# Performance work log

Measured on AMD Instinct MI355X. Metric: run time of the kernel, lower is better.

## Reference

```python
import jax, jax.numpy as jnp
import numpy as np

N_S, N_H, N_ACT, N_LINKS = 512, 256, 7, 9
AXIS_LIST = jnp.array([2, 0, 2, 2, 2, 0, 2])
LINK_LIST = jnp.arange(N_ACT)
ROT_SIGN = jnp.array([1., 1., 1., 1., -1., 1., 1.], dtype=jnp.float32)  # rot[..., 4] *= -1
MASS = jnp.array([105.98, 105.98, 314.98, 279.2, 105.98, 105.98, 243.66], dtype=jnp.float32)
TOTAL_MASS = jnp.sum(MASS) + 100000.0 + 243.66
DIAGS = jnp.array([[12.19, 12.19, 3.061], [12.19, 12.19, 3.061], [15.41, 2094.71, 2103.19],
                   [9.522, 1966.28, 1966.28], [8.305, 3.061, 8.0386], [12.13, 12.13, 3.061],
                   [9.336, 44.41, 44.41]], dtype=jnp.float32)
INERTIAL = DIAGS[:, :, None] * jnp.eye(3, dtype=jnp.float32)          # (7,3,3) diagonal inertias
SUM_MASS = jnp.cumsum(MASS[::-1])[::-1].reshape(1, 1, 1, N_ACT)       # suffix sums
SUM_INERTIAL = jnp.cumsum(INERTIAL[::-1], axis=0)[::-1]               # (7,3,3)
TRIL = jnp.tril(jnp.ones((N_ACT, N_ACT), dtype=jnp.float32)).reshape(1, 1, N_ACT, 1, N_ACT)
MASS_MASK = MASS.reshape(1, 1, N_ACT, 1, 1) * TRIL                    # mass_H_wphi_mask
TF0 = jnp.array([[1, 0, 0, 0], [0, -1, 0, 0], [0, 0, 1.3, 6], [0, 0, 0, 1]], dtype=jnp.float32)
COM0 = jnp.array([[1, 0, 0, 0], [0, 1, 0, 0], [0, 0, 1, 0.5], [0, 0, 0, 1]], dtype=jnp.float32)
BASE_COM = (TF0 @ COM0)[:3, 3] * 243.66 / (100000.0 + 243.66)


def _skew(p):
    x, y, z = p[..., 0], p[..., 1], p[..., 2]
    z0 = jnp.zeros_like(x)
    return jnp.stack([jnp.stack([z0, -z, y], -1),
                      jnp.stack([z, z0, -x], -1),
                      jnp.stack([-y, x, z0], -1)], -2)


def _skew_mul(p):
    x, y, z = p[..., 0], p[..., 1], p[..., 2]
    r2 = x * x + y * y + z * z
    row0 = jnp.stack([r2 - x * x, -x * y, -x * z], -1)
    row1 = jnp.stack([-x * y, r2 - y * y, -y * z], -1)
    row2 = jnp.stack([-x * z, -y * z, r2 - z * z], -1)
    return jnp.stack([row0, row1, row2], -2)


def _inv3(H):
    a, b, c = H[..., 0, 0], H[..., 0, 1], H[..., 0, 2]
    d, e, f = H[..., 1, 0], H[..., 1, 1], H[..., 1, 2]
    g, h, i = H[..., 2, 0], H[..., 2, 1], H[..., 2, 2]
    det = a * (e * i - f * h) - b * (d * i - f * g) + c * (d * h - e * g)
    C11 = e * i - f * h; C12 = -(b * i - c * h); C13 = b * f - c * e
    C21 = -(d * i - f * g); C22 = a * i - c * g; C23 = -(a * f - c * d)
    C31 = d * h - e * g; C32 = -(a * h - b * g); C33 = a * e - b * d
    adj = jnp.stack([jnp.stack([C11, C21, C31], -1),
                     jnp.stack([C12, C22, C32], -1),
                     jnp.stack([C13, C23, C33], -1)], -2)
    return adj / det[..., None, None]


def _forward(com_list, link_pose_list, bm):
    rot = link_pose_list[:, :, :3, AXIS_LIST, LINK_LIST] * ROT_SIGN  # (n,h,3,7)
    if bm:
        del_p = com_list[:, :, :, :N_ACT] - link_pose_list[:, :, :3, 3, :N_ACT]  # (n,h,3,7)
        del_p_a = jnp.swapaxes(del_p, -1, -2)                                     # (n,h,7,3)
        del_p_skew = _skew(del_p_a)                                               # (n,h,7,3,3)
        jacob_t = jnp.cross(rot, del_p, axis=2)                                   # (n,h,3,7)
        jacob_tw = jacob_t * SUM_MASS
        H_w = jnp.sum(INERTIAL.reshape(1, 1, N_ACT, 3, 3)
                      + MASS.reshape(1, 1, N_ACT, 1, 1) * _skew_mul(del_p_a), axis=2)  # (n,h,3,3)
        term1 = jnp.einsum('aij,shja->shia', SUM_INERTIAL, rot)                   # (n,h,3,7)
        jac_w = jacob_t[:, :, None] * MASS_MASK                                   # (n,h,7,3,7)
        term2 = jnp.einsum('shaij,shajk->shik', del_p_skew, jac_w)                # (n,h,3,7)
        H_wphi = term1 + term2
        system_com = jnp.einsum('ntci,i->ntc', com_list, MASS) / TOTAL_MASS       # (n,h,3)
        r_og = _skew(system_com - BASE_COM)                                       # (n,h,3,3)
        H_s = TOTAL_MASS * (r_og @ r_og) + H_w
        H_theta = H_wphi - r_og @ jacob_tw
        H_inv = _inv3(H_s)
        top = -(jacob_tw / TOTAL_MASS + r_og @ (H_inv @ H_theta))
        bot = -(H_inv @ H_theta)
        return jnp.concatenate([top, bot], axis=2)                                # (n,h,6,7)
    else:
        del_p = link_pose_list[:, :, :3, 3, -2][..., None] - link_pose_list[:, :, :3, 3, :N_ACT]
        jt = jnp.cross(rot, del_p, axis=2)
        return jnp.concatenate([jt, rot], axis=2)


def setup_inputs() -> dict:
    key = jax.random.key(0)
    k1, k2 = jax.random.split(key)
    com_list = jax.random.normal(k1, (N_S, N_H, 3, N_ACT), dtype=jnp.float32)
    link_pose_list = jax.random.normal(k2, (N_S, N_H, 4, 4, N_LINKS), dtype=jnp.float32)
    return {"com_list": com_list, "link_pose_list": link_pose_list, "bm": 1}


def reference(com_list, link_pose_list, bm):
    return _forward(com_list, link_pose_list, bm)
```

## Files before the change

kernel.cpp:

```cpp
#include <hip/hip_runtime.h>


#define BLK 256

__global__ __launch_bounds__(BLK) void canadarm_jacob_kernel(
    const float* __restrict__ com,
    const float* __restrict__ pose,
    const int* __restrict__ bm_ptr,
    float* __restrict__ out,
    int n_items)
{
    __shared__ float lds[BLK * 42];

    const int tid = threadIdx.x;
    const int idx = blockIdx.x * BLK + tid;

    const float MASS[7] = {105.98f, 105.98f, 314.98f, 279.2f, 105.98f, 105.98f, 243.66f};
    const float SUMM[7] = {1261.76f, 1155.78f, 1049.80f, 734.82f, 455.62f, 349.64f, 243.66f};
    const float SIX[7] = {79.083f, 66.893f, 54.703f, 39.293f, 29.771f, 21.466f, 9.336f};
    const float SIY[7] = {4144.971f, 4132.781f, 4120.591f, 2025.881f, 59.601f, 56.540f, 44.410f};
    const float SIZ[7] = {4131.1016f, 4128.0406f, 4124.9796f, 2021.7896f, 55.5096f, 47.471f, 44.410f};
    const float TM     = 101505.42f;
    const float INV_TM = 1.0f / 101505.42f;
    const float BCZ    = 6.65f * 243.66f / 100243.66f;

    {
        const float4* Cb4 = reinterpret_cast<const float4*>(com) + (size_t)blockIdx.x * (BLK * 21 / 4);
        float4* L4 = reinterpret_cast<float4*>(lds);
#pragma unroll
        for (int i = 0; i < 5; ++i) L4[tid + i * BLK] = Cb4[tid + i * BLK];
        if (tid < BLK * 21 / 4 - 5 * BLK) L4[tid + 5 * BLK] = Cb4[tid + 5 * BLK];
    }
    __syncthreads();

    const float4* Pb = reinterpret_cast<const float4*>(pose) + (size_t)idx * 36;
    float rot[3][7];
    float tr[3][8];
#pragma unroll
    for (int r = 0; r < 3; ++r) {
        const float4 q0 = Pb[r * 9 + 0];
        const float4 q1 = Pb[r * 9 + 1];
        const float4 q4 = Pb[r * 9 + 4];
        const float4 q5 = Pb[r * 9 + 5];
        const float4 q6 = Pb[r * 9 + 6];
        const float4 q7 = Pb[r * 9 + 7];
        const float4 q8 = Pb[r * 9 + 8];
        rot[r][0] = q4.z;
        rot[r][1] = q0.y;
        rot[r][2] = q5.x;
        rot[r][3] = q5.y;
        rot[r][4] = -q5.z;
        rot[r][5] = q1.y;
        rot[r][6] = q6.x;
        tr[r][0] = q6.w;
        tr[r][1] = q7.x; tr[r][2] = q7.y; tr[r][3] = q7.z; tr[r][4] = q7.w;
        tr[r][5] = q8.x; tr[r][6] = q8.y; tr[r][7] = q8.z;
    }

    const int bm = bm_ptr[0];
    float o[42];

    if (bm) {
        float cm[3][7];
#pragma unroll
        for (int r = 0; r < 3; ++r)
#pragma unroll
            for (int i = 0; i < 7; ++i) cm[r][i] = lds[tid * 21 + r * 7 + i];

        float scx = 0.f, scy = 0.f, scz = 0.f;
#pragma unroll
        for (int i = 0; i < 7; ++i) {
            scx += cm[0][i] * MASS[i];
            scy += cm[1][i] * MASS[i];
            scz += cm[2][i] * MASS[i];
        }
        const float vx = scx * INV_TM;
        const float vy = scy * INV_TM;
        const float vz = scz * INV_TM - BCZ;

        float dp[3][7], jt[3][7];
        float hxx = SIX[0], hyy = SIY[0], hzz = SIZ[0];
        float hxy = 0.f, hxz = 0.f, hyz = 0.f;
#pragma unroll
        for (int i = 0; i < 7; ++i) {
            const float x = cm[0][i] - tr[0][i];
            const float y = cm[1][i] - tr[1][i];
            const float z = cm[2][i] - tr[2][i];
            dp[0][i] = x; dp[1][i] = y; dp[2][i] = z;
            jt[0][i] = rot[1][i] * z - rot[2][i] * y;
            jt[1][i] = rot[2][i] * x - rot[0][i] * z;
            jt[2][i] = rot[0][i] * y - rot[1][i] * x;
            const float m = MASS[i];
            hxx += m * (y * y + z * z);
            hyy += m * (x * x + z * z);
            hzz += m * (x * x + y * y);
            hxy -= m * x * y;
            hxz -= m * x * z;
            hyz -= m * y * z;
        }

        float wx[7], wy[7], wz[7];
        wx[6] = MASS[6] * dp[0][6];
        wy[6] = MASS[6] * dp[1][6];
        wz[6] = MASS[6] * dp[2][6];
#pragma unroll
        for (int k = 5; k >= 0; --k) {
            wx[k] = wx[k + 1] + MASS[k] * dp[0][k];
            wy[k] = wy[k + 1] + MASS[k] * dp[1][k];
            wz[k] = wz[k + 1] + MASS[k] * dp[2][k];
        }

        const float vv = vx * vx + vy * vy + vz * vz;
        const float a  = hxx + TM * (vx * vx - vv);
        const float b  = hxy + TM * (vx * vy);
        const float c  = hxz + TM * (vx * vz);
        const float e  = hyy + TM * (vy * vy - vv);
        const float f  = hyz + TM * (vy * vz);
        const float i9 = hzz + TM * (vz * vz - vv);

        const float c11 = e * i9 - f * f;
        const float c12 = c * f - b * i9;
        const float c13 = b * f - e * c;
        const float det = a * c11 + b * c12 + c * c13;
        const float rdet = 1.0f / det;
        const float i00 = c11 * rdet;
        const float i01 = c12 * rdet;
        const float i02 = c13 * rdet;
        const float i11 = (a * i9 - c * c) * rdet;
        const float i12 = (c * b - a * f) * rdet;
        const float i22 = (a * e - b * b) * rdet;

#pragma unroll
        for (int k = 0; k < 7; ++k) {
            const float ux = wx[k] - SUMM[k] * vx;
            const float uy = wy[k] - SUMM[k] * vy;
            const float uz = wz[k] - SUMM[k] * vz;
            const float jx = jt[0][k], jy = jt[1][k], jz = jt[2][k];
            const float htx = SIX[k] * rot[0][k] + uy * jz - uz * jy;
            const float hty = SIY[k] * rot[1][k] + uz * jx - ux * jz;
            const float htz = SIZ[k] * rot[2][k] + ux * jy - uy * jx;
            const float bx = i00 * htx + i01 * hty + i02 * htz;
            const float by = i01 * htx + i11 * hty + i12 * htz;
            const float bz = i02 * htx + i12 * hty + i22 * htz;
            const float s = SUMM[k] * INV_TM;
            o[0 * 7 + k] = -(s * jx + vy * bz - vz * by);
            o[1 * 7 + k] = -(s * jy + vz * bx - vx * bz);
            o[2 * 7 + k] = -(s * jz + vx * by - vy * bx);
            o[3 * 7 + k] = -bx;
            o[4 * 7 + k] = -by;
            o[5 * 7 + k] = -bz;
        }
    } else {
#pragma unroll
        for (int k = 0; k < 7; ++k) {
            const float dx = tr[0][7] - tr[0][k];
            const float dy = tr[1][7] - tr[1][k];
            const float dz = tr[2][7] - tr[2][k];
            o[0 * 7 + k] = rot[1][k] * dz - rot[2][k] * dy;
            o[1 * 7 + k] = rot[2][k] * dx - rot[0][k] * dz;
            o[2 * 7 + k] = rot[0][k] * dy - rot[1][k] * dx;
            o[3 * 7 + k] = rot[0][k];
            o[4 * 7 + k] = rot[1][k];
            o[5 * 7 + k] = rot[2][k];
        }
    }

    __syncthreads();
#pragma unroll
    for (int j = 0; j < 42; ++j) lds[tid * 42 + j] = o[j];
    __syncthreads();

    {
        float4* Ob4 = reinterpret_cast<float4*>(out) + (size_t)blockIdx.x * (BLK * 42 / 4);
        const float4* L4 = reinterpret_cast<const float4*>(lds);
#pragma unroll
        for (int i = 0; i < 10; ++i) Ob4[tid + i * BLK] = L4[tid + i * BLK];
        if (tid < BLK * 42 / 4 - 10 * BLK) Ob4[tid + 10 * BLK] = L4[tid + 10 * BLK];
    }
}

extern "C" void kernel_launch(void* const* d_in, const int* in_sizes, int n_in,
                              void* d_out, int out_size, void* d_ws, size_t ws_size,
                              hipStream_t stream) {
    const float* com  = (const float*)d_in[0];
    const float* pose = (const float*)d_in[1];
    const int*   bm   = (const int*)d_in[2];
    float* out = (float*)d_out;

    const int n_items = in_sizes[0] / 21;
    const int grid = (n_items + BLK - 1) / BLK;
    canadarm_jacob_kernel<<<grid, BLK, 0, stream>>>(com, pose, bm, out, n_items);
}
```

Measured before the change: 125.8 us.

## Stage pose loads through LDS with coalesced reads, read com directly

The pose tensor is now loaded cooperatively. Each block of 128 threads reads contiguous float4s covering the first 28 of every item's 36 float4s, and only the 21 needed per item are kept in LDS. This replaces the strided per-thread 144-byte-stride gathers. The com data is now read directly per thread from global memory instead of being staged. The block size drops to 128 and the grid uses floor division, which assumes the item count is a multiple of 128.

```diff
diff --git a/kernel.cpp b/kernel.cpp
--- a/kernel.cpp
+++ b/kernel.cpp
@@ -1,7 +1,8 @@
 #include <hip/hip_runtime.h>
 
 
-#define BLK 256
+#define BLK 128
+#define IT_F4 23
 
 __global__ __launch_bounds__(BLK) void canadarm_jacob_kernel(
     const float* __restrict__ com,
@@ -10,10 +11,10 @@
     float* __restrict__ out,
     int n_items)
 {
-    __shared__ float lds[BLK * 42];
+    __shared__ float4 lds4[BLK * IT_F4];
 
     const int tid = threadIdx.x;
-    const int idx = blockIdx.x * BLK + tid;
+    const int item0 = blockIdx.x * BLK;
 
     const float MASS[7] = {105.98f, 105.98f, 314.98f, 279.2f, 105.98f, 105.98f, 243.66f};
     const float SUMM[7] = {1261.76f, 1155.78f, 1049.80f, 734.82f, 455.62f, 349.64f, 243.66f};
@@ -25,26 +26,34 @@
     const float BCZ    = 6.65f * 243.66f / 100243.66f;
 
     {
-        const float4* Cb4 = reinterpret_cast<const float4*>(com) + (size_t)blockIdx.x * (BLK * 21 / 4);
-        float4* L4 = reinterpret_cast<float4*>(lds);
-#pragma unroll
-        for (int i = 0; i < 5; ++i) L4[tid + i * BLK] = Cb4[tid + i * BLK];
-        if (tid < BLK * 21 / 4 - 5 * BLK) L4[tid + 5 * BLK] = Cb4[tid + 5 * BLK];
+        const float4* Pb = reinterpret_cast<const float4*>(pose) + (size_t)item0 * 36;
+#pragma unroll
+        for (int it = 0; it < 28; ++it) {
+            const int c = it * BLK + tid;
+            const int item = c / 28;
+            const int off = c - item * 28;
+            const float4 v = Pb[item * 36 + off];
+            const int r = off / 9;
+            const int oo = off - r * 9;
+            const bool live = (r < 3) && (oo < 2 || oo >= 4);
+            const int slot = 7 * r + (oo < 2 ? oo : oo - 2);
+            if (live) lds4[item * IT_F4 + slot] = v;
+        }
     }
     __syncthreads();
 
-    const float4* Pb = reinterpret_cast<const float4*>(pose) + (size_t)idx * 36;
+    const float4* L = &lds4[tid * IT_F4];
     float rot[3][7];
     float tr[3][8];
 #pragma unroll
     for (int r = 0; r < 3; ++r) {
-        const float4 q0 = Pb[r * 9 + 0];
-        const float4 q1 = Pb[r * 9 + 1];
-        const float4 q4 = Pb[r * 9 + 4];
-        const float4 q5 = Pb[r * 9 + 5];
-        const float4 q6 = Pb[r * 9 + 6];
-        const float4 q7 = Pb[r * 9 + 7];
-        const float4 q8 = Pb[r * 9 + 8];
+        const float4 q0 = L[7 * r + 0];
+        const float4 q1 = L[7 * r + 1];
+        const float4 q4 = L[7 * r + 2];
+        const float4 q5 = L[7 * r + 3];
+        const float4 q6 = L[7 * r + 4];
+        const float4 q7 = L[7 * r + 5];
+        const float4 q8 = L[7 * r + 6];
         rot[r][0] = q4.z;
         rot[r][1] = q0.y;
         rot[r][2] = q5.x;
@@ -61,11 +70,12 @@
     float o[42];
 
     if (bm) {
+        const float* C = com + (size_t)(item0 + tid) * 21;
         float cm[3][7];
 #pragma unroll
         for (int r = 0; r < 3; ++r)
 #pragma unroll
-            for (int i = 0; i < 7; ++i) cm[r][i] = lds[tid * 21 + r * 7 + i];
+            for (int i = 0; i < 7; ++i) cm[r][i] = C[r * 7 + i];
 
         float scx = 0.f, scy = 0.f, scz = 0.f;
 #pragma unroll
@@ -166,16 +176,18 @@
     }
 
     __syncthreads();
-#pragma unroll
-    for (int j = 0; j < 42; ++j) lds[tid * 42 + j] = o[j];
+    float* ldsf = reinterpret_cast<float*>(lds4);
+#pragma unroll
+    for (int j = 0; j < 42; ++j) ldsf[tid * 42 + j] = o[j];
     __syncthreads();
 
     {
         float4* Ob4 = reinterpret_cast<float4*>(out) + (size_t)blockIdx.x * (BLK * 42 / 4);
-        const float4* L4 = reinterpret_cast<const float4*>(lds);
-#pragma unroll
-        for (int i = 0; i < 10; ++i) Ob4[tid + i * BLK] = L4[tid + i * BLK];
-        if (tid < BLK * 42 / 4 - 10 * BLK) Ob4[tid + 10 * BLK] = L4[tid + 10 * BLK];
+        const float4* Lf4 = reinterpret_cast<const float4*>(ldsf);
+#pragma unroll
+        for (int i = 0; i < 10; ++i) Ob4[tid + i * BLK] = Lf4[tid + i * BLK];
+        if (tid < BLK * 42 / 4 - 10 * BLK)
+            Ob4[tid + 10 * BLK] = Lf4[tid + 10 * BLK];
     }
 }
 
@@ -188,6 +200,6 @@
     float* out = (float*)d_out;
 
     const int n_items = in_sizes[0] / 21;
-    const int grid = (n_items + BLK - 1) / BLK;
+    const int grid = n_items / BLK;
     canadarm_jacob_kernel<<<grid, BLK, 0, stream>>>(com, pose, bm, out, n_items);
 }
```

New measurement: 149.1 us. 1.19x slower.
